# Performance work log

Measured on AMD Instinct MI355X. Metric: run time of the kernel, lower is better.

## Reference

```python
import jax, jax.numpy as jnp
import numpy as np

T = 1024  # output_length
H = 15    # GRU hidden size
I = 10    # seed size
O = 128   # output_size
B = 512   # batch

def setup_inputs() -> dict:
    key = jax.random.key(0)
    ks = jax.random.split(key, 8)
    s = 1.0 / np.sqrt(H)
    return {
        "feed": jax.random.normal(ks[0], (B, 1, I), dtype=jnp.float32),
        "h0":   jax.random.uniform(ks[1], (B, H), dtype=jnp.float32),
        "W_ih": jax.random.normal(ks[2], (3 * H, I), dtype=jnp.float32) * s,
        "W_hh": jax.random.normal(ks[3], (3 * H, H), dtype=jnp.float32) * s,
        "b_ih": jax.random.normal(ks[4], (3 * H,), dtype=jnp.float32) * s,
        "b_hh": jax.random.normal(ks[5], (3 * H,), dtype=jnp.float32) * s,
        "W_out": jax.random.normal(ks[6], (O, H), dtype=jnp.float32) * s,
        "b_out": jnp.zeros((O,), dtype=jnp.float32),
    }

def reference(feed, h0, W_ih, W_hh, b_ih, b_hh, W_out, b_out):
    # feed is repeated along time in the original, so the input-gate
    # projection is identical at every step: compute it once.
    x = feed[:, 0, :]                         # [B, I]
    gi = x @ W_ih.T + b_ih                    # [B, 3H]
    i_r, i_z, i_n = jnp.split(gi, 3, axis=-1)  # torch GRU gate order: r, z, n

    def step(h, _):
        gh = h @ W_hh.T + b_hh                # [B, 3H]
        h_r, h_z, h_n = jnp.split(gh, 3, axis=-1)
        r = jax.nn.sigmoid(i_r + h_r)
        z = jax.nn.sigmoid(i_z + h_z)
        n = jnp.tanh(i_n + r * h_n)
        h_new = (1.0 - z) * n + z * h
        return h_new, h_new

    _, hs = jax.lax.scan(step, h0, None, length=T)  # [T, B, H]
    # Linear + sigmoid; original returns output.transpose(0,1) -> [T, B, O],
    # which scan's time-major layout already gives us.
    out = jax.nn.sigmoid(jnp.einsum("tbh,oh->tbo", hs, W_out) + b_out)
    return out
```

## Files before the change

kernel.cpp:

```cpp
#include <hip/hip_runtime.h>
#include <cstdint>

#define Tt 1024
#define Hh 15
#define Ii 10
#define Oo 128
#define Bb 512

typedef float v4f __attribute__((ext_vector_type(4)));

__device__ __forceinline__ float sigmoidf_(float x) {
    return 1.0f / (1.0f + __expf(-x));
}
__device__ __forceinline__ float tanhf_(float x) {
    return 1.0f - 2.0f / (__expf(2.0f * x) + 1.0f);
}

#define ROT(x, j) __int_as_float(__builtin_amdgcn_update_dpp( \
    0, __float_as_int(x), 0x120 + (j), 0xF, 0xF, true))

__global__ __launch_bounds__(64, 1) void gru_recur(
    const float* __restrict__ feed, const float* __restrict__ h0,
    const float* __restrict__ W_ih, const float* __restrict__ W_hh,
    const float* __restrict__ b_ih, const float* __restrict__ b_hh,
    float* __restrict__ hs)
{
    const int lane = threadIdx.x;
    const int g = lane >> 4;
    const int u = lane & 15;
    const int uu = (u < Hh) ? u : 0;
    const int b = blockIdx.x * 4 + g;

    int pr = __builtin_amdgcn_update_dpp(0, lane & 15, 0x121, 0xF, 0xF, true);
    int p0 = __builtin_amdgcn_readfirstlane(pr);
    const int dir = (p0 == 1) ? 1 : 15;

    float Wr[16], Wz[16], Wn[16];
    #pragma unroll
    for (int j = 0; j < 16; ++j) {
        int k = (uu + dir * j) & 15;
        bool ok = (k < Hh);
        int kk = ok ? k : 0;
        Wr[j] = ok ? W_hh[(uu         ) * Hh + kk] : 0.0f;
        Wz[j] = ok ? W_hh[(uu +     Hh) * Hh + kk] : 0.0f;
        Wn[j] = ok ? W_hh[(uu + 2 * Hh) * Hh + kk] : 0.0f;
    }

    float cr = b_ih[uu]          + b_hh[uu];
    float cz = b_ih[uu + Hh]     + b_hh[uu + Hh];
    float cn = b_ih[uu + 2 * Hh];
    float bn = b_hh[uu + 2 * Hh];
    #pragma unroll
    for (int i = 0; i < Ii; ++i) {
        float x = feed[b * Ii + i];
        cr += x * W_ih[(uu         ) * Ii + i];
        cz += x * W_ih[(uu +     Hh) * Ii + i];
        cn += x * W_ih[(uu + 2 * Hh) * Ii + i];
    }

    float hcur = (u < Hh) ? h0[b * Hh + uu] : 0.0f;
    size_t off = (size_t)b * 16 + u;

    for (int t = 0; t < Tt; ++t) {
        float hr[16];
        hr[0]  = hcur;
        hr[1]  = ROT(hcur, 1);   hr[2]  = ROT(hcur, 2);
        hr[3]  = ROT(hcur, 3);   hr[4]  = ROT(hcur, 4);
        hr[5]  = ROT(hcur, 5);   hr[6]  = ROT(hcur, 6);
        hr[7]  = ROT(hcur, 7);   hr[8]  = ROT(hcur, 8);
        hr[9]  = ROT(hcur, 9);   hr[10] = ROT(hcur, 10);
        hr[11] = ROT(hcur, 11);  hr[12] = ROT(hcur, 12);
        hr[13] = ROT(hcur, 13);  hr[14] = ROT(hcur, 14);
        hr[15] = ROT(hcur, 15);

        float ar[4] = {cr, 0.f, 0.f, 0.f};
        float az[4] = {cz, 0.f, 0.f, 0.f};
        float an[4] = {bn, 0.f, 0.f, 0.f};
        #pragma unroll
        for (int j = 0; j < 16; ++j) {
            ar[j & 3] += Wr[j] * hr[j];
            az[j & 3] += Wz[j] * hr[j];
            an[j & 3] += Wn[j] * hr[j];
        }
        float r = sigmoidf_((ar[0] + ar[1]) + (ar[2] + ar[3]));
        float z = sigmoidf_((az[0] + az[1]) + (az[2] + az[3]));
        float dn = (an[0] + an[1]) + (an[2] + an[3]);
        float n = tanhf_(cn + r * dn);
        float hnew = n + z * (hcur - n);

        hs[off] = hnew;
        off += (size_t)Bb * 16;
        hcur = hnew;
    }
}

__device__ __forceinline__ v4f ntload4(const float* p) {
    return __builtin_nontemporal_load((const v4f*)p);
}

__global__ __launch_bounds__(256) void gru_proj(
    const float* __restrict__ hs, const float* __restrict__ W_out,
    const float* __restrict__ b_out, float* __restrict__ out)
{
    const int q  = threadIdx.x & 31;
    const int gg = threadIdx.x >> 5;
    const int o0 = q * 4;

    float w[4][Hh];
    float bo[4];
    #pragma unroll
    for (int j = 0; j < 4; ++j) {
        bo[j] = b_out[o0 + j];
        #pragma unroll
        for (int k = 0; k < Hh; ++k) w[j][k] = W_out[(o0 + j) * Hh + k];
    }

    const int P = Tt * Bb;
    const int stride = gridDim.x * 8;
    int p = blockIdx.x * 8 + gg;
    if (p >= P) return;

    const float* hp = hs + (size_t)p * 16;
    v4f A = ntload4(hp), B_ = ntload4(hp + 4), C = ntload4(hp + 8), D = ntload4(hp + 12);

    while (true) {
        int pn = p + stride;
        bool more = pn < P;
        const float* hpn = hs + (size_t)(more ? pn : p) * 16;
        v4f A2 = ntload4(hpn), B2 = ntload4(hpn + 4),
            C2 = ntload4(hpn + 8), D2 = ntload4(hpn + 12);

        float h[Hh] = {A.x, A.y, A.z, A.w, B_.x, B_.y, B_.z, B_.w,
                       C.x, C.y, C.z, C.w, D.x, D.y, D.z};
        float acc[4];
        #pragma unroll
        for (int j = 0; j < 4; ++j) {
            float s0 = bo[j], s1 = 0.f;
            #pragma unroll
            for (int k = 0; k < Hh; k += 2) s0 += h[k] * w[j][k];
            #pragma unroll
            for (int k = 1; k < Hh; k += 2) s1 += h[k] * w[j][k];
            acc[j] = sigmoidf_(s0 + s1);
        }
        v4f res = {acc[0], acc[1], acc[2], acc[3]};
        __builtin_nontemporal_store(res, (v4f*)(out + (size_t)p * (size_t)Oo + o0));

        if (!more) break;
        p = pn; A = A2; B_ = B2; C = C2; D = D2;
    }
}

extern "C" void kernel_launch(void* const* d_in, const int* in_sizes, int n_in,
                              void* d_out, int out_size, void* d_ws, size_t ws_size,
                              hipStream_t stream) {
    const float* feed  = (const float*)d_in[0];
    const float* h0    = (const float*)d_in[1];
    const float* W_ih  = (const float*)d_in[2];
    const float* W_hh  = (const float*)d_in[3];
    const float* b_ih  = (const float*)d_in[4];
    const float* b_hh  = (const float*)d_in[5];
    const float* W_out = (const float*)d_in[6];
    const float* b_out = (const float*)d_in[7];
    float* out = (float*)d_out;
    float* hs  = (float*)d_ws;

    gru_recur<<<Bb / 4, 64, 0, stream>>>(feed, h0, W_ih, W_hh, b_ih, b_hh, hs);
    gru_proj<<<2048, 256, 0, stream>>>(hs, W_out, b_out, out);
}
```

Measured before the change: 526.9 us.

## Fuse recurrence and projection into one persistent kernel with chunked flag signalling

Merges the GRU recurrence and output projection into one launch. Atomic tickets assign the first 32 blocks to run the recurrence (16 batch rows each). The remaining 1024 blocks each project one timestep, spin-waiting on per-128-step chunk counters stored in the workspace. This lets the projection overlap with the serial recurrence instead of waiting for it to finish. It relies on producer blocks being scheduled before consumers; padded lanes are redirected to write into the control area, and a memset is added to clear the counters.

```diff
diff --git a/kernel.cpp b/kernel.cpp
--- a/kernel.cpp
+++ b/kernel.cpp
@@ -6,6 +6,10 @@
 #define Ii 10
 #define Oo 128
 #define Bb 512
+
+#define NPROD 32
+#define CH    128
+#define NSIG  128
 
 typedef float v4f __attribute__((ext_vector_type(4)));
 
@@ -19,134 +23,158 @@
 #define ROT(x, j) __int_as_float(__builtin_amdgcn_update_dpp( \
     0, __float_as_int(x), 0x120 + (j), 0xF, 0xF, true))
 
-__global__ __launch_bounds__(64, 1) void gru_recur(
-    const float* __restrict__ feed, const float* __restrict__ h0,
-    const float* __restrict__ W_ih, const float* __restrict__ W_hh,
-    const float* __restrict__ b_ih, const float* __restrict__ b_hh,
-    float* __restrict__ hs)
-{
-    const int lane = threadIdx.x;
-    const int g = lane >> 4;
-    const int u = lane & 15;
-    const int uu = (u < Hh) ? u : 0;
-    const int b = blockIdx.x * 4 + g;
-
-    int pr = __builtin_amdgcn_update_dpp(0, lane & 15, 0x121, 0xF, 0xF, true);
-    int p0 = __builtin_amdgcn_readfirstlane(pr);
-    const int dir = (p0 == 1) ? 1 : 15;
-
-    float Wr[16], Wz[16], Wn[16];
-    #pragma unroll
-    for (int j = 0; j < 16; ++j) {
-        int k = (uu + dir * j) & 15;
-        bool ok = (k < Hh);
-        int kk = ok ? k : 0;
-        Wr[j] = ok ? W_hh[(uu         ) * Hh + kk] : 0.0f;
-        Wz[j] = ok ? W_hh[(uu +     Hh) * Hh + kk] : 0.0f;
-        Wn[j] = ok ? W_hh[(uu + 2 * Hh) * Hh + kk] : 0.0f;
-    }
-
-    float cr = b_ih[uu]          + b_hh[uu];
-    float cz = b_ih[uu + Hh]     + b_hh[uu + Hh];
-    float cn = b_ih[uu + 2 * Hh];
-    float bn = b_hh[uu + 2 * Hh];
-    #pragma unroll
-    for (int i = 0; i < Ii; ++i) {
-        float x = feed[b * Ii + i];
-        cr += x * W_ih[(uu         ) * Ii + i];
-        cz += x * W_ih[(uu +     Hh) * Ii + i];
-        cn += x * W_ih[(uu + 2 * Hh) * Ii + i];
-    }
-
-    float hcur = (u < Hh) ? h0[b * Hh + uu] : 0.0f;
-    size_t off = (size_t)b * 16 + u;
-
-    for (int t = 0; t < Tt; ++t) {
-        float hr[16];
-        hr[0]  = hcur;
-        hr[1]  = ROT(hcur, 1);   hr[2]  = ROT(hcur, 2);
-        hr[3]  = ROT(hcur, 3);   hr[4]  = ROT(hcur, 4);
-        hr[5]  = ROT(hcur, 5);   hr[6]  = ROT(hcur, 6);
-        hr[7]  = ROT(hcur, 7);   hr[8]  = ROT(hcur, 8);
-        hr[9]  = ROT(hcur, 9);   hr[10] = ROT(hcur, 10);
-        hr[11] = ROT(hcur, 11);  hr[12] = ROT(hcur, 12);
-        hr[13] = ROT(hcur, 13);  hr[14] = ROT(hcur, 14);
-        hr[15] = ROT(hcur, 15);
-
-        float ar[4] = {cr, 0.f, 0.f, 0.f};
-        float az[4] = {cz, 0.f, 0.f, 0.f};
-        float an[4] = {bn, 0.f, 0.f, 0.f};
-        #pragma unroll
-        for (int j = 0; j < 16; ++j) {
-            ar[j & 3] += Wr[j] * hr[j];
-            az[j & 3] += Wz[j] * hr[j];
-            an[j & 3] += Wn[j] * hr[j];
-        }
-        float r = sigmoidf_((ar[0] + ar[1]) + (ar[2] + ar[3]));
-        float z = sigmoidf_((az[0] + az[1]) + (az[2] + az[3]));
-        float dn = (an[0] + an[1]) + (an[2] + an[3]);
-        float n = tanhf_(cn + r * dn);
-        float hnew = n + z * (hcur - n);
-
-        hs[off] = hnew;
-        off += (size_t)Bb * 16;
-        hcur = hnew;
-    }
-}
-
 __device__ __forceinline__ v4f ntload4(const float* p) {
     return __builtin_nontemporal_load((const v4f*)p);
 }
 
-__global__ __launch_bounds__(256) void gru_proj(
-    const float* __restrict__ hs, const float* __restrict__ W_out,
-    const float* __restrict__ b_out, float* __restrict__ out)
+__global__ __launch_bounds__(256) void gru_fused(
+    const float* __restrict__ feed, const float* __restrict__ h0,
+    const float* __restrict__ W_ih, const float* __restrict__ W_hh,
+    const float* __restrict__ b_ih, const float* __restrict__ b_hh,
+    const float* __restrict__ W_out, const float* __restrict__ b_out,
+    float* __restrict__ out, float* __restrict__ hs)
 {
-    const int q  = threadIdx.x & 31;
-    const int gg = threadIdx.x >> 5;
-    const int o0 = q * 4;
+    int* ctl = (int*)hs;
+    __shared__ int s_ticket;
+    if (threadIdx.x == 0)
+        s_ticket = atomicAdd(ctl + 15, 1);
+    __syncthreads();
+    const int bt = s_ticket;
+    const int tid = threadIdx.x;
 
-    float w[4][Hh];
-    float bo[4];
-    #pragma unroll
-    for (int j = 0; j < 4; ++j) {
-        bo[j] = b_out[o0 + j];
+    if (bt < NPROD) {
+        const int lane = tid & 63;
+        const int wv   = tid >> 6;
+        const int g    = lane >> 4;
+        const int u    = lane & 15;
+        const int uu   = (u < Hh) ? u : 0;
+        const int b    = bt * 16 + wv * 4 + g;
+
+        int pr = __builtin_amdgcn_update_dpp(0, lane & 15, 0x121, 0xF, 0xF, true);
+        int p0 = __builtin_amdgcn_readfirstlane(pr);
+        const int dir = (p0 == 1) ? 1 : 15;
+
+        float Wr[16], Wz[16], Wn[16];
         #pragma unroll
-        for (int k = 0; k < Hh; ++k) w[j][k] = W_out[(o0 + j) * Hh + k];
-    }
+        for (int j = 0; j < 16; ++j) {
+            int k = (uu + dir * j) & 15;
+            bool ok = (k < Hh);
+            int kk = ok ? k : 0;
+            Wr[j] = ok ? W_hh[(uu         ) * Hh + kk] : 0.0f;
+            Wz[j] = ok ? W_hh[(uu +     Hh) * Hh + kk] : 0.0f;
+            Wn[j] = ok ? W_hh[(uu + 2 * Hh) * Hh + kk] : 0.0f;
+        }
 
-    const int P = Tt * Bb;
-    const int stride = gridDim.x * 8;
-    int p = blockIdx.x * 8 + gg;
-    if (p >= P) return;
+        float cr = b_ih[uu]          + b_hh[uu];
+        float cz = b_ih[uu + Hh]     + b_hh[uu + Hh];
+        float cn = b_ih[uu + 2 * Hh];
+        float bn = b_hh[uu + 2 * Hh];
+        #pragma unroll
+        for (int i = 0; i < Ii; ++i) {
+            float x = feed[b * Ii + i];
+            cr += x * W_ih[(uu         ) * Ii + i];
+            cz += x * W_ih[(uu +     Hh) * Ii + i];
+            cn += x * W_ih[(uu + 2 * Hh) * Ii + i];
+        }
 
-    const float* hp = hs + (size_t)p * 16;
-    v4f A = ntload4(hp), B_ = ntload4(hp + 4), C = ntload4(hp + 8), D = ntload4(hp + 12);
+        float hcur = (u < Hh) ? h0[b * Hh + uu] : 0.0f;
+        size_t off = (u < Hh) ? ((size_t)b * 16 + u)
+                              : ((size_t)(64 + (b & 255)) * 16 + 15);
 
-    while (true) {
-        int pn = p + stride;
-        bool more = pn < P;
-        const float* hpn = hs + (size_t)(more ? pn : p) * 16;
-        v4f A2 = ntload4(hpn), B2 = ntload4(hpn + 4),
-            C2 = ntload4(hpn + 8), D2 = ntload4(hpn + 12);
+        for (int t = 0; t < Tt; ++t) {
+            float hr[16];
+            hr[0]  = hcur;
+            hr[1]  = ROT(hcur, 1);   hr[2]  = ROT(hcur, 2);
+            hr[3]  = ROT(hcur, 3);   hr[4]  = ROT(hcur, 4);
+            hr[5]  = ROT(hcur, 5);   hr[6]  = ROT(hcur, 6);
+            hr[7]  = ROT(hcur, 7);   hr[8]  = ROT(hcur, 8);
+            hr[9]  = ROT(hcur, 9);   hr[10] = ROT(hcur, 10);
+            hr[11] = ROT(hcur, 11);  hr[12] = ROT(hcur, 12);
+            hr[13] = ROT(hcur, 13);  hr[14] = ROT(hcur, 14);
+            hr[15] = ROT(hcur, 15);
 
-        float h[Hh] = {A.x, A.y, A.z, A.w, B_.x, B_.y, B_.z, B_.w,
-                       C.x, C.y, C.z, C.w, D.x, D.y, D.z};
-        float acc[4];
+            float ar[4] = {cr, 0.f, 0.f, 0.f};
+            float az[4] = {cz, 0.f, 0.f, 0.f};
+            float an[4] = {bn, 0.f, 0.f, 0.f};
+            #pragma unroll
+            for (int j = 0; j < 16; ++j) {
+                ar[j & 3] += Wr[j] * hr[j];
+                az[j & 3] += Wz[j] * hr[j];
+                an[j & 3] += Wn[j] * hr[j];
+            }
+            float r = sigmoidf_((ar[0] + ar[1]) + (ar[2] + ar[3]));
+            float z = sigmoidf_((az[0] + az[1]) + (az[2] + az[3]));
+            float dn = (an[0] + an[1]) + (an[2] + an[3]);
+            float n = tanhf_(cn + r * dn);
+            float hnew = n + z * (hcur - n);
+
+            hs[off] = hnew;
+            off += (size_t)Bb * 16;
+            hcur = hnew;
+
+            if ((t & (CH - 1)) == (CH - 1)) {
+                __threadfence();
+                if ((tid & 63) == 0)
+                    atomicAdd(ctl + (1 + (t >> 7)) * 16 + 15, 1);
+            }
+        }
+    } else {
+        const int t  = bt - NPROD;
+        const int q  = tid & 31;
+        const int gg = tid >> 5;
+        const int o0 = q * 4;
+
+        float w[4][Hh];
+        float bo[4];
         #pragma unroll
         for (int j = 0; j < 4; ++j) {
-            float s0 = bo[j], s1 = 0.f;
+            bo[j] = b_out[o0 + j];
             #pragma unroll
-            for (int k = 0; k < Hh; k += 2) s0 += h[k] * w[j][k];
+            for (int k = 0; k < Hh; ++k) w[j][k] = W_out[(o0 + j) * Hh + k];
+        }
+
+        int* done = ctl + (1 + (t >> 7)) * 16 + 15;
+        if (tid == 0) {
+            while (__hip_atomic_load(done, __ATOMIC_RELAXED,
+                                     __HIP_MEMORY_SCOPE_AGENT) < NSIG)
+                __builtin_amdgcn_s_sleep(32);
+        }
+        __syncthreads();
+        __threadfence();
+
+        const float* base  = hs  + (size_t)t * (Bb * 16);
+        float*       obase = out + (size_t)t * ((size_t)Bb * Oo);
+
+        int b = gg;
+        const float* hp = base + (size_t)b * 16;
+        v4f A = ntload4(hp), B_ = ntload4(hp + 4),
+            C = ntload4(hp + 8), D = ntload4(hp + 12);
+
+        #pragma unroll 2
+        for (int it = 0; it < Bb / 8; ++it) {
+            int bnx = b + 8;
+            bool more = (it < Bb / 8 - 1);
+            const float* hq = base + (size_t)(more ? bnx : b) * 16;
+            v4f A2 = ntload4(hq), B2 = ntload4(hq + 4),
+                C2 = ntload4(hq + 8), D2 = ntload4(hq + 12);
+
+            float h[Hh] = {A.x, A.y, A.z, A.w, B_.x, B_.y, B_.z, B_.w,
+                           C.x, C.y, C.z, C.w, D.x, D.y, D.z};
+            float acc[4];
             #pragma unroll
-            for (int k = 1; k < Hh; k += 2) s1 += h[k] * w[j][k];
-            acc[j] = sigmoidf_(s0 + s1);
+            for (int j = 0; j < 4; ++j) {
+                float s0 = bo[j], s1 = 0.f;
+                #pragma unroll
+                for (int k = 0; k < Hh; k += 2) s0 += h[k] * w[j][k];
+                #pragma unroll
+                for (int k = 1; k < Hh; k += 2) s1 += h[k] * w[j][k];
+                acc[j] = sigmoidf_(s0 + s1);
+            }
+            v4f res = {acc[0], acc[1], acc[2], acc[3]};
+            __builtin_nontemporal_store(res, (v4f*)(obase + (size_t)b * Oo + o0));
+
+            b = bnx; A = A2; B_ = B2; C = C2; D = D2;
         }
-        v4f res = {acc[0], acc[1], acc[2], acc[3]};
-        __builtin_nontemporal_store(res, (v4f*)(out + (size_t)p * (size_t)Oo + o0));
-
-        if (!more) break;
-        p = pn; A = A2; B_ = B2; C = C2; D = D2;
     }
 }
 
@@ -164,6 +192,7 @@
     float* out = (float*)d_out;
     float* hs  = (float*)d_ws;
 
-    gru_recur<<<Bb / 4, 64, 0, stream>>>(feed, h0, W_ih, W_hh, b_ih, b_hh, hs);
-    gru_proj<<<2048, 256, 0, stream>>>(hs, W_out, b_out, out);
+    hipMemsetAsync(d_ws, 0, 1024, stream);
+    gru_fused<<<NPROD + Tt, 256, 0, stream>>>(
+        feed, h0, W_ih, W_hh, b_ih, b_hh, W_out, b_out, out, hs);
 }
```

Result: slower. 905.3 us (+71.8%).

## Fuse output projection into GRU recurrence kernel, dropping hidden-state workspace

Applied to the files above, without the earlier changes.

Merges the separate projection kernel into the recurrent kernel. Each lane computes 8 of the 128 outputs per timestep from the DPP-rotated hidden state, using packed v2f FMAs, and stores them directly. This removes the hs workspace write and re-read and the second launch. The cost is that the output projection, its sigmoids and the stores now sit on the serial recurrence path. Only 128 single-wave blocks run, so the 268MB output write may be limited by low parallelism.

```diff
diff --git a/kernel.cpp b/kernel.cpp
--- a/kernel.cpp
+++ b/kernel.cpp
@@ -8,6 +8,7 @@
 #define Bb 512
 
 typedef float v4f __attribute__((ext_vector_type(4)));
+typedef float v2f __attribute__((ext_vector_type(2)));
 
 __device__ __forceinline__ float sigmoidf_(float x) {
     return 1.0f / (1.0f + __expf(-x));
@@ -19,11 +20,23 @@
 #define ROT(x, j) __int_as_float(__builtin_amdgcn_update_dpp( \
     0, __float_as_int(x), 0x120 + (j), 0xF, 0xF, true))
 
-__global__ __launch_bounds__(64, 1) void gru_recur(
+#define ROTALL(dst, src)                                        \
+    dst[0]  = (src);                                            \
+    dst[1]  = ROT(src, 1);   dst[2]  = ROT(src, 2);             \
+    dst[3]  = ROT(src, 3);   dst[4]  = ROT(src, 4);             \
+    dst[5]  = ROT(src, 5);   dst[6]  = ROT(src, 6);             \
+    dst[7]  = ROT(src, 7);   dst[8]  = ROT(src, 8);             \
+    dst[9]  = ROT(src, 9);   dst[10] = ROT(src, 10);            \
+    dst[11] = ROT(src, 11);  dst[12] = ROT(src, 12);            \
+    dst[13] = ROT(src, 13);  dst[14] = ROT(src, 14);            \
+    dst[15] = ROT(src, 15);
+
+__global__ __launch_bounds__(64, 1) void gru_fused(
     const float* __restrict__ feed, const float* __restrict__ h0,
     const float* __restrict__ W_ih, const float* __restrict__ W_hh,
     const float* __restrict__ b_ih, const float* __restrict__ b_hh,
-    float* __restrict__ hs)
+    const float* __restrict__ W_out, const float* __restrict__ b_out,
+    float* __restrict__ out)
 {
     const int lane = threadIdx.x;
     const int g = lane >> 4;
@@ -46,6 +59,26 @@
         Wn[j] = ok ? W_hh[(uu + 2 * Hh) * Hh + kk] : 0.0f;
     }
 
+    v2f Wo[8][8];
+    float bo[8];
+    #pragma unroll
+    for (int m = 0; m < 8; ++m) {
+        bo[m] = b_out[u * 8 + m];
+        #pragma unroll
+        for (int jp = 0; jp < 8; ++jp) {
+            float w0, w1;
+            {
+                int k = (u + dir * (2 * jp)) & 15;
+                w0 = (k < Hh) ? W_out[(u * 8 + m) * Hh + k] : 0.0f;
+            }
+            {
+                int k = (u + dir * (2 * jp + 1)) & 15;
+                w1 = (k < Hh) ? W_out[(u * 8 + m) * Hh + k] : 0.0f;
+            }
+            Wo[m][jp] = (v2f){w0, w1};
+        }
+    }
+
     float cr = b_ih[uu]          + b_hh[uu];
     float cz = b_ih[uu + Hh]     + b_hh[uu + Hh];
     float cn = b_ih[uu + 2 * Hh];
@@ -59,20 +92,13 @@
     }
 
     float hcur = (u < Hh) ? h0[b * Hh + uu] : 0.0f;
-    size_t off = (size_t)b * 16 + u;
+
+    float hr[16];
+    ROTALL(hr, hcur);
+
+    float* op = out + (size_t)b * Oo + (size_t)u * 8;
 
     for (int t = 0; t < Tt; ++t) {
-        float hr[16];
-        hr[0]  = hcur;
-        hr[1]  = ROT(hcur, 1);   hr[2]  = ROT(hcur, 2);
-        hr[3]  = ROT(hcur, 3);   hr[4]  = ROT(hcur, 4);
-        hr[5]  = ROT(hcur, 5);   hr[6]  = ROT(hcur, 6);
-        hr[7]  = ROT(hcur, 7);   hr[8]  = ROT(hcur, 8);
-        hr[9]  = ROT(hcur, 9);   hr[10] = ROT(hcur, 10);
-        hr[11] = ROT(hcur, 11);  hr[12] = ROT(hcur, 12);
-        hr[13] = ROT(hcur, 13);  hr[14] = ROT(hcur, 14);
-        hr[15] = ROT(hcur, 15);
-
         float ar[4] = {cr, 0.f, 0.f, 0.f};
         float az[4] = {cz, 0.f, 0.f, 0.f};
         float an[4] = {bn, 0.f, 0.f, 0.f};
@@ -88,65 +114,29 @@
         float n = tanhf_(cn + r * dn);
         float hnew = n + z * (hcur - n);
 
-        hs[off] = hnew;
-        off += (size_t)Bb * 16;
+        ROTALL(hr, hnew);
         hcur = hnew;
-    }
-}
 
-__device__ __forceinline__ v4f ntload4(const float* p) {
-    return __builtin_nontemporal_load((const v4f*)p);
-}
+        v2f h2[8];
+        #pragma unroll
+        for (int jp = 0; jp < 8; ++jp)
+            h2[jp] = (v2f){hr[2 * jp], hr[2 * jp + 1]};
 
-__global__ __launch_bounds__(256) void gru_proj(
-    const float* __restrict__ hs, const float* __restrict__ W_out,
-    const float* __restrict__ b_out, float* __restrict__ out)
-{
-    const int q  = threadIdx.x & 31;
-    const int gg = threadIdx.x >> 5;
-    const int o0 = q * 4;
+        float o8[8];
+        #pragma unroll
+        for (int m = 0; m < 8; ++m) {
+            v2f a = (v2f){bo[m], 0.0f};
+            #pragma unroll
+            for (int jp = 0; jp < 8; ++jp)
+                a += Wo[m][jp] * h2[jp];
+            o8[m] = sigmoidf_(a.x + a.y);
+        }
 
-    float w[4][Hh];
-    float bo[4];
-    #pragma unroll
-    for (int j = 0; j < 4; ++j) {
-        bo[j] = b_out[o0 + j];
-        #pragma unroll
-        for (int k = 0; k < Hh; ++k) w[j][k] = W_out[(o0 + j) * Hh + k];
-    }
-
-    const int P = Tt * Bb;
-    const int stride = gridDim.x * 8;
-    int p = blockIdx.x * 8 + gg;
-    if (p >= P) return;
-
-    const float* hp = hs + (size_t)p * 16;
-    v4f A = ntload4(hp), B_ = ntload4(hp + 4), C = ntload4(hp + 8), D = ntload4(hp + 12);
-
-    while (true) {
-        int pn = p + stride;
-        bool more = pn < P;
-        const float* hpn = hs + (size_t)(more ? pn : p) * 16;
-        v4f A2 = ntload4(hpn), B2 = ntload4(hpn + 4),
-            C2 = ntload4(hpn + 8), D2 = ntload4(hpn + 12);
-
-        float h[Hh] = {A.x, A.y, A.z, A.w, B_.x, B_.y, B_.z, B_.w,
-                       C.x, C.y, C.z, C.w, D.x, D.y, D.z};
-        float acc[4];
-        #pragma unroll
-        for (int j = 0; j < 4; ++j) {
-            float s0 = bo[j], s1 = 0.f;
-            #pragma unroll
-            for (int k = 0; k < Hh; k += 2) s0 += h[k] * w[j][k];
-            #pragma unroll
-            for (int k = 1; k < Hh; k += 2) s1 += h[k] * w[j][k];
-            acc[j] = sigmoidf_(s0 + s1);
-        }
-        v4f res = {acc[0], acc[1], acc[2], acc[3]};
-        __builtin_nontemporal_store(res, (v4f*)(out + (size_t)p * (size_t)Oo + o0));
-
-        if (!more) break;
-        p = pn; A = A2; B_ = B2; C = C2; D = D2;
+        v4f lo = {o8[0], o8[1], o8[2], o8[3]};
+        v4f hi = {o8[4], o8[5], o8[6], o8[7]};
+        __builtin_nontemporal_store(lo, (v4f*)op);
+        __builtin_nontemporal_store(hi, (v4f*)(op + 4));
+        op += (size_t)Bb * Oo;
     }
 }
 
@@ -162,8 +152,8 @@
     const float* W_out = (const float*)d_in[6];
     const float* b_out = (const float*)d_in[7];
     float* out = (float*)d_out;
-    float* hs  = (float*)d_ws;
+    (void)d_ws;
 
-    gru_recur<<<Bb / 4, 64, 0, stream>>>(feed, h0, W_ih, W_hh, b_ih, b_hh, hs);
-    gru_proj<<<2048, 256, 0, stream>>>(hs, W_out, b_out, out);
+    gru_fused<<<Bb / 4, 64, 0, stream>>>(
+        feed, h0, W_ih, W_hh, b_ih, b_hh, W_out, b_out, out);
 }
```

Result: slower. 856.4 us (+62.5%).

## Split GRU gates across wave rows, one batch per wave, with packed FMA

Applied to the files above, without the earlier changes.

Each wave now handles one batch element instead of four. The three gate matvecs are spread across 16-lane rows, and results are gathered with shuffles. The per-lane dot product uses packed two-wide float FMAs over eight pairs, which shortens the serial dependency chain per timestep. This adds a cross-row shuffle (ds_bpermute) each step, quadruples the block count to 512 waves, and leaves the fourth row doing redundant work.

```diff
diff --git a/kernel.cpp b/kernel.cpp
--- a/kernel.cpp
+++ b/kernel.cpp
@@ -8,6 +8,7 @@
 #define Bb 512
 
 typedef float v4f __attribute__((ext_vector_type(4)));
+typedef float v2f __attribute__((ext_vector_type(2)));
 
 __device__ __forceinline__ float sigmoidf_(float x) {
     return 1.0f / (1.0f + __expf(-x));
@@ -26,24 +27,29 @@
     float* __restrict__ hs)
 {
     const int lane = threadIdx.x;
-    const int g = lane >> 4;
-    const int u = lane & 15;
-    const int uu = (u < Hh) ? u : 0;
-    const int b = blockIdx.x * 4 + g;
+    const int row  = lane >> 4;
+    const int u    = lane & 15;
+    const int uu   = (u < Hh) ? u : 0;
+    const int gate = (row < 3) ? row : 0;
+    const int b    = blockIdx.x;
 
     int pr = __builtin_amdgcn_update_dpp(0, lane & 15, 0x121, 0xF, 0xF, true);
     int p0 = __builtin_amdgcn_readfirstlane(pr);
     const int dir = (p0 == 1) ? 1 : 15;
 
-    float Wr[16], Wz[16], Wn[16];
+    v2f Wp[8];
     #pragma unroll
-    for (int j = 0; j < 16; ++j) {
-        int k = (uu + dir * j) & 15;
-        bool ok = (k < Hh);
-        int kk = ok ? k : 0;
-        Wr[j] = ok ? W_hh[(uu         ) * Hh + kk] : 0.0f;
-        Wz[j] = ok ? W_hh[(uu +     Hh) * Hh + kk] : 0.0f;
-        Wn[j] = ok ? W_hh[(uu + 2 * Hh) * Hh + kk] : 0.0f;
+    for (int jp = 0; jp < 8; ++jp) {
+        float w0 = 0.0f, w1 = 0.0f;
+        {
+            int k = (uu + dir * (2 * jp)) & 15;
+            if (u < Hh && k < Hh) w0 = W_hh[(uu + gate * Hh) * Hh + k];
+        }
+        {
+            int k = (uu + dir * (2 * jp + 1)) & 15;
+            if (u < Hh && k < Hh) w1 = W_hh[(uu + gate * Hh) * Hh + k];
+        }
+        Wp[jp] = (v2f){w0, w1};
     }
 
     float cr = b_ih[uu]          + b_hh[uu];
@@ -57,38 +63,41 @@
         cz += x * W_ih[(uu +     Hh) * Ii + i];
         cn += x * W_ih[(uu + 2 * Hh) * Ii + i];
     }
+    const float seed = (gate == 0) ? cr : (gate == 1) ? cz : bn;
 
     float hcur = (u < Hh) ? h0[b * Hh + uu] : 0.0f;
     size_t off = (size_t)b * 16 + u;
 
     for (int t = 0; t < Tt; ++t) {
-        float hr[16];
-        hr[0]  = hcur;
-        hr[1]  = ROT(hcur, 1);   hr[2]  = ROT(hcur, 2);
-        hr[3]  = ROT(hcur, 3);   hr[4]  = ROT(hcur, 4);
-        hr[5]  = ROT(hcur, 5);   hr[6]  = ROT(hcur, 6);
-        hr[7]  = ROT(hcur, 7);   hr[8]  = ROT(hcur, 8);
-        hr[9]  = ROT(hcur, 9);   hr[10] = ROT(hcur, 10);
-        hr[11] = ROT(hcur, 11);  hr[12] = ROT(hcur, 12);
-        hr[13] = ROT(hcur, 13);  hr[14] = ROT(hcur, 14);
-        hr[15] = ROT(hcur, 15);
+        v2f h2[8];
+        h2[0].x = hcur;          h2[0].y = ROT(hcur, 1);
+        h2[1].x = ROT(hcur, 2);  h2[1].y = ROT(hcur, 3);
+        h2[2].x = ROT(hcur, 4);  h2[2].y = ROT(hcur, 5);
+        h2[3].x = ROT(hcur, 6);  h2[3].y = ROT(hcur, 7);
+        h2[4].x = ROT(hcur, 8);  h2[4].y = ROT(hcur, 9);
+        h2[5].x = ROT(hcur, 10); h2[5].y = ROT(hcur, 11);
+        h2[6].x = ROT(hcur, 12); h2[6].y = ROT(hcur, 13);
+        h2[7].x = ROT(hcur, 14); h2[7].y = ROT(hcur, 15);
 
-        float ar[4] = {cr, 0.f, 0.f, 0.f};
-        float az[4] = {cz, 0.f, 0.f, 0.f};
-        float an[4] = {bn, 0.f, 0.f, 0.f};
-        #pragma unroll
-        for (int j = 0; j < 16; ++j) {
-            ar[j & 3] += Wr[j] * hr[j];
-            az[j & 3] += Wz[j] * hr[j];
-            an[j & 3] += Wn[j] * hr[j];
-        }
-        float r = sigmoidf_((ar[0] + ar[1]) + (ar[2] + ar[3]));
-        float z = sigmoidf_((az[0] + az[1]) + (az[2] + az[3]));
-        float dn = (an[0] + an[1]) + (an[2] + an[3]);
-        float n = tanhf_(cn + r * dn);
+        v2f a0 = (v2f){seed, 0.0f};
+        v2f a1 = (v2f){0.0f, 0.0f};
+        a0 += Wp[0] * h2[0];  a1 += Wp[1] * h2[1];
+        a0 += Wp[2] * h2[2];  a1 += Wp[3] * h2[3];
+        a0 += Wp[4] * h2[4];  a1 += Wp[5] * h2[5];
+        a0 += Wp[6] * h2[6];  a1 += Wp[7] * h2[7];
+        v2f s2 = a0 + a1;
+        float a = s2.x + s2.y;
+
+        float ga_r = __shfl(a, u);
+        float ga_z = __shfl(a, u + 16);
+        float ga_n = __shfl(a, u + 32);
+
+        float r = sigmoidf_(ga_r);
+        float z = sigmoidf_(ga_z);
+        float n = tanhf_(cn + r * ga_n);
         float hnew = n + z * (hcur - n);
 
-        hs[off] = hnew;
+        if (lane < 16) hs[off] = hnew;
         off += (size_t)Bb * 16;
         hcur = hnew;
     }
@@ -164,6 +173,6 @@
     float* out = (float*)d_out;
     float* hs  = (float*)d_ws;
 
-    gru_recur<<<Bb / 4, 64, 0, stream>>>(feed, h0, W_ih, W_hh, b_ih, b_hh, hs);
+    gru_recur<<<Bb, 64, 0, stream>>>(feed, h0, W_ih, W_hh, b_ih, b_hh, hs);
     gru_proj<<<2048, 256, 0, stream>>>(hs, W_out, b_out, out);
 }
```

After: 573.9 us. +8.9%, slower.
